# Kernel optimization log

Measured on AMD Instinct MI355X. Metric: run time of the kernel, lower is better.

Reference implementation:

```python
import jax, jax.numpy as jnp
import numpy as np

B, T, C = 4, 8192, 1024
H, D = 16, 64  # n_head, head_dim


def setup_inputs() -> dict:
    key = jax.random.key(0)
    ks = jax.random.split(key, 9)
    s = 1.0 / np.sqrt(C)
    return {
        "x": jax.random.normal(ks[0], (B, T, C), jnp.float32),
        "Wq": jax.random.uniform(ks[1], (C, C), jnp.float32, -s, s),
        "bq": jax.random.uniform(ks[2], (C,), jnp.float32, -s, s),
        "Wk": jax.random.uniform(ks[3], (C, C), jnp.float32, -s, s),
        "bk": jax.random.uniform(ks[4], (C,), jnp.float32, -s, s),
        "Wv": jax.random.uniform(ks[5], (C, C), jnp.float32, -s, s),
        "bv": jax.random.uniform(ks[6], (C,), jnp.float32, -s, s),
        "Wp": jax.random.uniform(ks[7], (C, C), jnp.float32, -s, s),
        "bp": jax.random.uniform(ks[8], (C,), jnp.float32, -s, s),
    }


def _heads(t):
    # (B,T,C) -> (B,H,T,D)
    return t.reshape(B, T, H, D).transpose(0, 2, 1, 3)


def reference(x, Wq, bq, Wk, bk, Wv, bv, Wp, bp):
    q = _heads(x @ Wq.T + bq)
    k = _heads(x @ Wk.T + bk)
    v = _heads(x @ Wv.T + bv)
    # attn_type='l1': softmax q,k over feature dim; L1 normalizer
    q = jax.nn.softmax(q, axis=-1)
    k = jax.nn.softmax(k, axis=-1)
    k_sum = k.sum(axis=-2, keepdims=True)               # (B,H,1,D)
    D_inv = 1.0 / (q * k_sum).sum(axis=-1, keepdims=True)  # (B,H,T,1)
    context = jnp.einsum('bhtd,bhte->bhde', k, v)       # (B,H,D,D)
    out = jnp.einsum('bhtd,bhde->bhte', q, context) * D_inv + q
    out = out.transpose(0, 2, 1, 3).reshape(B, T, C)
    return out @ Wp.T + bp
```

## Files before the change

kernel.cpp:

```cpp
#include <hip/hip_runtime.h>
#include <hip/hip_bf16.h>
#include <stdint.h>


#define BT    32768
#define CDIM  1024

using bf16 = __hip_bfloat16;
typedef short  short8   __attribute__((ext_vector_type(8)));
typedef short  short4_t __attribute__((ext_vector_type(4)));
typedef unsigned short ushort4_t __attribute__((ext_vector_type(4)));
typedef float  floatx4  __attribute__((ext_vector_type(4)));

__device__ __forceinline__ float bfbits2f(unsigned short u) {
    union { unsigned int i; float f; } c; c.i = ((unsigned int)u) << 16; return c.f;
}

__device__ __forceinline__ void gld_lds16(const void* g, void* lds) {
    __builtin_amdgcn_global_load_lds(
        (const __attribute__((address_space(1))) uint32_t*)g,
        (__attribute__((address_space(3))) uint32_t*)lds,
        16, 0, 0);
}

__global__ void zero_kernel(float* __restrict__ p) {
    p[(size_t)blockIdx.x * 256 + threadIdx.x] = 0.0f;
}

__global__ void cvt_kernel(const float* __restrict__ x,
                           const float* __restrict__ Wq, const float* __restrict__ Wk,
                           const float* __restrict__ Wv, const float* __restrict__ Wp,
                           bf16* __restrict__ xb, bf16* __restrict__ Wb) {
    const int XF4 = (BT * CDIM) / 4;
    int i = blockIdx.x * 256 + threadIdx.x;
    const float* src; bf16* dst; int off;
    if (i < XF4) { src = x; dst = xb; off = i; }
    else {
        int i2 = i - XF4;
        int wi = i2 >> 18;
        off = i2 & 0x3FFFF;
        src = (wi == 0) ? Wq : (wi == 1) ? Wk : (wi == 2) ? Wv : Wp;
        dst = Wb + (size_t)wi * 1048576;
    }
    float4 f = ((const float4*)src)[off];
    union { bf16 h[4]; short4_t v; } u;
    u.h[0] = __float2bfloat16(f.x); u.h[1] = __float2bfloat16(f.y);
    u.h[2] = __float2bfloat16(f.z); u.h[3] = __float2bfloat16(f.w);
    *(short4_t*)(dst + (size_t)off * 4) = u.v;
}


__device__ __forceinline__ short8 frag_ld(const bf16* hb, int r, int s4q) {
    return *(const short8*)(hb + r * 64 + (((s4q) ^ (r & 7)) << 3));
}

__device__ __forceinline__ void stage_half(const bf16* g, bf16* l, int tid) {
    int ln = tid & 63, w = tid >> 6;
    int r = w * 8 + (ln >> 3);
    int c = ((ln & 7) ^ (ln >> 3)) << 3;
    gld_lds16(g + (size_t)r * CDIM + c, l + w * 512);
    gld_lds16(g + (size_t)(r + 64) * CDIM + c, l + 4096 + w * 512);
}

#define MFMA16(a, b, c) __builtin_amdgcn_mfma_f32_16x16x32_bf16(a, b, c, 0, 0, 0)

__device__ __forceinline__ void pipe256(const bf16* __restrict__ Ab,
                                        const bf16* __restrict__ Bb,
                                        bf16* ldsA, bf16* ldsB,
                                        int tid, floatx4 acc[8][4]) {
    const int lane = tid & 63;
    const int wv = tid >> 6;
    const int quad = lane >> 4, l15 = lane & 15;
    const int wm = wv >> 2, wn = wv & 3;
    const int rA0 = wm * 64 + l15;
    const int rB0 = (wn & 1) * 64 + l15;
    const bf16* ldsBh = ldsB + (wn >> 1) * 8192;
    short8 bfr[4][2];

#define STAGE_A(b, h, kt) stage_half(Ab + (size_t)((h) * 128) * CDIM + (kt) * 64, \
                                     ldsA + (b) * 16384 + (h) * 8192, tid)
#define STAGE_B(b, h, kt) stage_half(Bb + (size_t)((h) * 128) * CDIM + (kt) * 64, \
                                     ldsB + (b) * 16384 + (h) * 8192, tid)
#define VMW(n) asm volatile("s_waitcnt vmcnt(" #n ")" ::: "memory")
#define VM_NONE

#define QPHASE(BUF, QA, MM, LOADB, STG, VMC) do {                              \
    const bf16* aH_ = ldsA + (BUF) * 16384 + (QA) * 8192;                      \
    short8 a00_ = frag_ld(aH_, rA0 + (MM) * 32,      quad);                    \
    short8 a01_ = frag_ld(aH_, rA0 + (MM) * 32,      4 + quad);                \
    short8 a10_ = frag_ld(aH_, rA0 + (MM) * 32 + 16, quad);                    \
    short8 a11_ = frag_ld(aH_, rA0 + (MM) * 32 + 16, 4 + quad);                \
    if (LOADB) {                                                               \
        const bf16* bH_ = ldsBh + (BUF) * 16384;                               \
        _Pragma("unroll")                                                      \
        for (int j = 0; j < 4; ++j) {                                          \
            bfr[j][0] = frag_ld(bH_, rB0 + j * 16, quad);                      \
            bfr[j][1] = frag_ld(bH_, rB0 + j * 16, 4 + quad);                  \
        }                                                                      \
    }                                                                          \
    STG; VMC;                                                                  \
    __builtin_amdgcn_s_barrier();                                              \
    asm volatile("s_waitcnt lgkmcnt(0)" ::: "memory");                         \
    __builtin_amdgcn_s_setprio(1);                                             \
    _Pragma("unroll")                                                          \
    for (int j = 0; j < 4; ++j) {                                              \
        acc[(QA)*4+(MM)*2  ][j] = MFMA16(a00_, bfr[j][0], acc[(QA)*4+(MM)*2  ][j]); \
        acc[(QA)*4+(MM)*2  ][j] = MFMA16(a01_, bfr[j][1], acc[(QA)*4+(MM)*2  ][j]); \
        acc[(QA)*4+(MM)*2+1][j] = MFMA16(a10_, bfr[j][0], acc[(QA)*4+(MM)*2+1][j]); \
        acc[(QA)*4+(MM)*2+1][j] = MFMA16(a11_, bfr[j][1], acc[(QA)*4+(MM)*2+1][j]); \
    }                                                                          \
    __builtin_amdgcn_s_setprio(0);                                             \
    __builtin_amdgcn_s_barrier();                                              \
} while (0)

    STAGE_B(0, 0, 0); STAGE_B(0, 1, 0); STAGE_A(0, 0, 0); STAGE_A(0, 1, 0);
    STAGE_B(1, 0, 1); STAGE_B(1, 1, 1); STAGE_A(1, 0, 1);
    VMW(8);
    __builtin_amdgcn_s_barrier();

    #pragma unroll 1
    for (int i = 0; i < 7; ++i) {
        int t = 2 * i;
        QPHASE(0, 0, 0, 1, STAGE_A(1, 1, t + 1), VM_NONE);
        QPHASE(0, 0, 1, 0, STAGE_B(0, 0, t + 2), VMW(10));
        QPHASE(0, 1, 0, 0, STAGE_B(0, 1, t + 2), VM_NONE);
        QPHASE(0, 1, 1, 0, STAGE_A(0, 0, t + 2), VMW(8));
        QPHASE(1, 0, 0, 1, STAGE_A(0, 1, t + 2), VM_NONE);
        QPHASE(1, 0, 1, 0, STAGE_B(1, 0, t + 3), VMW(10));
        QPHASE(1, 1, 0, 0, STAGE_B(1, 1, t + 3), VM_NONE);
        QPHASE(1, 1, 1, 0, STAGE_A(1, 0, t + 3), VMW(8));
    }
    QPHASE(0, 0, 0, 1, STAGE_A(1, 1, 15), VM_NONE);
    QPHASE(0, 0, 1, 0, VM_NONE, VMW(8));
    QPHASE(0, 1, 0, 0, VM_NONE, VM_NONE);
    QPHASE(0, 1, 1, 0, VM_NONE, VMW(2));
    QPHASE(1, 0, 0, 1, VM_NONE, VM_NONE);
    QPHASE(1, 0, 1, 0, VM_NONE, VMW(0));
    QPHASE(1, 1, 0, 0, VM_NONE, VM_NONE);
    QPHASE(1, 1, 1, 0, VM_NONE, VM_NONE);

#undef QPHASE
#undef STAGE_A
#undef STAGE_B
}

__global__ __launch_bounds__(512, 2)
void gemm_qkv(const bf16* __restrict__ A, const bf16* __restrict__ Bw,
              const float* __restrict__ bq, const float* __restrict__ bk,
              const float* __restrict__ bv,
              bf16* __restrict__ qb, bf16* __restrict__ kb, bf16* __restrict__ vb) {
    __shared__ bf16 ldsA[32768];
    __shared__ bf16 ldsB[32768];
    int tid = threadIdx.x;
    int bid = blockIdx.x;
    int swz = (bid & 7) * 192 + (bid >> 3);
    int bn = swz % 12, bm = swz / 12;

    floatx4 acc[8][4] = {};
    pipe256(A + (size_t)bm * 256 * CDIM, Bw + (size_t)bn * 256 * CDIM,
            ldsA, ldsB, tid, acc);

    int lane = tid & 63, wv = tid >> 6, quad = lane >> 4, l15 = lane & 15;
    int wm = wv >> 2, wn = wv & 3;
    int n_abs = bn * 256 + wn * 64;
    bf16* dst; const float* biasp; int ncol0; bool smax;
    if (n_abs < 1024)      { dst = qb; biasp = bq; ncol0 = n_abs;        smax = true;  }
    else if (n_abs < 2048) { dst = kb; biasp = bk; ncol0 = n_abs - 1024; smax = true;  }
    else                   { dst = vb; biasp = bv; ncol0 = n_abs - 2048; smax = false; }
    float bias4[4];
    #pragma unroll
    for (int j = 0; j < 4; ++j) bias4[j] = biasp[ncol0 + j * 16 + l15];
    size_t row0 = (size_t)bm * 256 + wm * 64;

    #pragma unroll
    for (int i = 0; i < 8; ++i) {
        #pragma unroll
        for (int r = 0; r < 4; ++r) {
            float vals[4];
            #pragma unroll
            for (int j = 0; j < 4; ++j) vals[j] = acc[i][j][r] + bias4[j];
            if (smax) {
                float mx = fmaxf(fmaxf(vals[0], vals[1]), fmaxf(vals[2], vals[3]));
                #pragma unroll
                for (int d = 1; d < 16; d <<= 1) mx = fmaxf(mx, __shfl_xor(mx, d));
                float s = 0.f;
                #pragma unroll
                for (int j = 0; j < 4; ++j) { vals[j] = __expf(vals[j] - mx); s += vals[j]; }
                #pragma unroll
                for (int d = 1; d < 16; d <<= 1) s += __shfl_xor(s, d);
                float rinv = 1.0f / s;
                #pragma unroll
                for (int j = 0; j < 4; ++j) vals[j] *= rinv;
            }
            size_t row = row0 + ((i >> 2) * 128) + ((i & 3) * 16) + quad * 4 + r;
            #pragma unroll
            for (int j = 0; j < 4; ++j)
                dst[row * 1024 + ncol0 + j * 16 + l15] = __float2bfloat16(vals[j]);
        }
    }
}

__global__ __launch_bounds__(256)
void ctx_kernel(const bf16* __restrict__ kbuf, const bf16* __restrict__ vbuf,
                float* __restrict__ ctx, float* __restrict__ ksum) {
    int bid = blockIdx.x;
    int head = bid >> 4, chunk = bid & 15;
    int b = head >> 4, h = head & 15;
    size_t rowbase = (size_t)b * 8192 + (size_t)chunk * 512;
    int coff = h * 64;
    __shared__ bf16 ks[64 * 64];
    __shared__ bf16 vs[64 * 64];
    int tid = threadIdx.x;
    int lrow = tid >> 2, lpart = tid & 3;
    int di = tid >> 4, ei = tid & 15;

    float acc[16];
    #pragma unroll
    for (int i = 0; i < 16; ++i) acc[i] = 0.f;
    float ksv[4] = {0.f, 0.f, 0.f, 0.f};

    size_t gbase = (rowbase + lrow) * 1024 + coff + lpart * 16;
    short8 pk0 = *(const short8*)(kbuf + gbase);
    short8 pk1 = *(const short8*)(kbuf + gbase + 8);
    short8 pv0 = *(const short8*)(vbuf + gbase);
    short8 pv1 = *(const short8*)(vbuf + gbase + 8);

    for (int st = 0; st < 8; ++st) {
        __syncthreads();
        *(short8*)&ks[lrow * 64 + lpart * 16]     = pk0;
        *(short8*)&ks[lrow * 64 + lpart * 16 + 8] = pk1;
        *(short8*)&vs[lrow * 64 + lpart * 16]     = pv0;
        *(short8*)&vs[lrow * 64 + lpart * 16 + 8] = pv1;
        __syncthreads();
        if (st < 7) {
            size_t g = gbase + (size_t)(st + 1) * 64 * 1024;
            pk0 = *(const short8*)(kbuf + g);
            pk1 = *(const short8*)(kbuf + g + 8);
            pv0 = *(const short8*)(vbuf + g);
            pv1 = *(const short8*)(vbuf + g + 8);
        }
        for (int t = 0; t < 64; ++t) {
            ushort4_t ku = *(const ushort4_t*)&ks[t * 64 + di * 4];
            ushort4_t vu = *(const ushort4_t*)&vs[t * 64 + ei * 4];
            float kd[4], ve[4];
            #pragma unroll
            for (int i = 0; i < 4; ++i) { kd[i] = bfbits2f(ku[i]); ve[i] = bfbits2f(vu[i]); }
            #pragma unroll
            for (int i = 0; i < 4; ++i)
                #pragma unroll
                for (int j = 0; j < 4; ++j)
                    acc[i * 4 + j] = fmaf(kd[i], ve[j], acc[i * 4 + j]);
            #pragma unroll
            for (int j = 0; j < 4; ++j) ksv[j] += kd[j];
        }
    }
    float* cptr = ctx + (size_t)head * 4096;
    #pragma unroll
    for (int i = 0; i < 4; ++i)
        #pragma unroll
        for (int j = 0; j < 4; ++j)
            atomicAdd(&cptr[(di * 4 + i) * 64 + ei * 4 + j], acc[i * 4 + j]);
    if (ei == 0) {
        #pragma unroll
        for (int j = 0; j < 4; ++j) atomicAdd(&ksum[head * 64 + di * 4 + j], ksv[j]);
    }
}

#define QS 72
__global__ __launch_bounds__(256)
void attn_kernel(const bf16* __restrict__ qbuf, const float* __restrict__ ctx,
                 const float* __restrict__ ksum, bf16* __restrict__ ab) {
    int bid = blockIdx.x;
    int head = bid >> 7, tb = bid & 127;
    int b = head >> 4, h = head & 15;
    size_t row0 = (size_t)b * 8192 + (size_t)tb * 64;
    int coff = h * 64;
    __shared__ bf16 qs[64 * QS];
    __shared__ bf16 cts[64 * QS];
    __shared__ float ksums[64];
    __shared__ float dinv[64];
    int tid = threadIdx.x, lane = tid & 63, wv = tid >> 6;

    {
        int lrow = tid >> 2, lpart = tid & 3;
        size_t g = (row0 + lrow) * 1024 + coff + lpart * 16;
        short8 q0 = *(const short8*)(qbuf + g);
        short8 q1 = *(const short8*)(qbuf + g + 8);
        *(short8*)&qs[lrow * QS + lpart * 16]     = q0;
        *(short8*)&qs[lrow * QS + lpart * 16 + 8] = q1;
    }
    {
        const float* cp = ctx + (size_t)head * 4096;
        #pragma unroll
        for (int it = 0; it < 4; ++it) {
            int fi = it * 256 + tid;
            int d = fi >> 4, e0 = (fi & 15) * 4;
            float4 f = ((const float4*)cp)[fi];
            cts[(e0 + 0) * QS + d] = __float2bfloat16(f.x);
            cts[(e0 + 1) * QS + d] = __float2bfloat16(f.y);
            cts[(e0 + 2) * QS + d] = __float2bfloat16(f.z);
            cts[(e0 + 3) * QS + d] = __float2bfloat16(f.w);
        }
    }
    if (tid < 64) ksums[tid] = ksum[head * 64 + tid];
    __syncthreads();

    {
        int t = tid >> 2, dg = tid & 3;
        float p = 0.f;
        #pragma unroll
        for (int j = 0; j < 16; ++j)
            p = fmaf(__bfloat162float(qs[t * QS + dg * 16 + j]), ksums[dg * 16 + j], p);
        p += __shfl_xor(p, 1);
        p += __shfl_xor(p, 2);
        if (dg == 0) dinv[t] = 1.0f / p;
    }
    __syncthreads();

    int quad = lane >> 4, l15 = lane & 15;
    int trow0 = wv * 16;
    short8 aF0 = *(const short8*)&qs[(trow0 + l15) * QS + quad * 8];
    short8 aF1 = *(const short8*)&qs[(trow0 + l15) * QS + 32 + quad * 8];
    floatx4 acc[4] = {};
    #pragma unroll
    for (int ni = 0; ni < 4; ++ni) {
        short8 b0 = *(const short8*)&cts[(ni * 16 + l15) * QS + quad * 8];
        short8 b1 = *(const short8*)&cts[(ni * 16 + l15) * QS + 32 + quad * 8];
        acc[ni] = __builtin_amdgcn_mfma_f32_16x16x32_bf16(aF0, b0, acc[ni], 0, 0, 0);
        acc[ni] = __builtin_amdgcn_mfma_f32_16x16x32_bf16(aF1, b1, acc[ni], 0, 0, 0);
    }
    float dv[4];
    #pragma unroll
    for (int r = 0; r < 4; ++r) dv[r] = dinv[trow0 + quad * 4 + r];
    #pragma unroll
    for (int ni = 0; ni < 4; ++ni) {
        #pragma unroll
        for (int r = 0; r < 4; ++r) {
            int row = trow0 + quad * 4 + r;
            int col = ni * 16 + l15;
            float val = acc[ni][r] * dv[r] + __bfloat162float(qs[row * QS + col]);
            ab[(row0 + row) * 1024 + coff + col] = __float2bfloat16(val);
        }
    }
}

__global__ __launch_bounds__(512, 2)
void gemm_out(const bf16* __restrict__ A, const bf16* __restrict__ Bw,
              const float* __restrict__ bp, float* __restrict__ outp) {
    __shared__ bf16 ldsA[32768];
    __shared__ bf16 ldsB[32768];
    int tid = threadIdx.x;
    int bid = blockIdx.x;
    int swz = (bid & 7) * 64 + (bid >> 3);
    int bn = swz & 3, bm = swz >> 2;

    floatx4 acc[8][4] = {};
    pipe256(A + (size_t)bm * 256 * CDIM, Bw + (size_t)bn * 256 * CDIM,
            ldsA, ldsB, tid, acc);

    int lane = tid & 63, wv = tid >> 6, quad = lane >> 4, l15 = lane & 15;
    int wm = wv >> 2, wn = wv & 3;
    int gcol0 = bn * 256 + wn * 64;
    float bias4[4];
    #pragma unroll
    for (int j = 0; j < 4; ++j) bias4[j] = bp[gcol0 + j * 16 + l15];
    size_t row0 = (size_t)bm * 256 + wm * 64;

    #pragma unroll
    for (int i = 0; i < 8; ++i) {
        #pragma unroll
        for (int r = 0; r < 4; ++r) {
            size_t row = row0 + ((i >> 2) * 128) + ((i & 3) * 16) + quad * 4 + r;
            #pragma unroll
            for (int j = 0; j < 4; ++j)
                outp[row * 1024 + gcol0 + j * 16 + l15] = acc[i][j][r] + bias4[j];
        }
    }
}

extern "C" void kernel_launch(void* const* d_in, const int* in_sizes, int n_in,
                              void* d_out, int out_size, void* d_ws, size_t ws_size,
                              hipStream_t stream) {
    const float* x  = (const float*)d_in[0];
    const float* Wq = (const float*)d_in[1];
    const float* bq = (const float*)d_in[2];
    const float* Wk = (const float*)d_in[3];
    const float* bk = (const float*)d_in[4];
    const float* Wv = (const float*)d_in[5];
    const float* bv = (const float*)d_in[6];
    const float* Wp = (const float*)d_in[7];
    const float* bp = (const float*)d_in[8];
    float* outp = (float*)d_out;

    char* ws = (char*)d_ws;
    bf16*  xb   = (bf16*)(ws);
    bf16*  Wb   = (bf16*)(ws + 67108864);
    bf16*  qb   = (bf16*)(ws + 75497472);
    bf16*  kb   = (bf16*)(ws + 142606336);
    bf16*  vb   = (bf16*)(ws + 209715200);
    float* ctx  = (float*)(ws + 276824064);
    float* ksum = (float*)(ws + 277872640);
    bf16*  ab   = (bf16*)(ws);

    zero_kernel<<<1040, 256, 0, stream>>>(ctx);
    cvt_kernel<<<36864, 256, 0, stream>>>(x, Wq, Wk, Wv, Wp, xb, Wb);
    gemm_qkv<<<1536, 512, 0, stream>>>(xb, Wb, bq, bk, bv, qb, kb, vb);
    ctx_kernel<<<1024, 256, 0, stream>>>(kb, vb, ctx, ksum);
    attn_kernel<<<8192, 256, 0, stream>>>(qb, ctx, ksum, ab);
    gemm_out<<<512, 512, 0, stream>>>(ab, Wb + (size_t)3072 * 1024, bp, outp);
}
```

Before: 691.3 us.

## Compute K^T V context with MFMA via transposed swizzled LDS tiles

The context kernel previously computed the per-head D×D K^T·V outer-product sum with scalar FMAs on bf16 values read from LDS. It now stores K and V tiles transposed (d-major) in LDS with an XOR swizzle and uses 16x16x32 bf16 MFMA instructions to accumulate the context, with the k_sum reduction folded into the staging loop and reduced through shuffles and a shared buffer. This removes scalar FMA and LDS-read overhead, at the cost of scalar 2-byte transposed LDS writes and more complex indexing. The gemm_out kernel and macros are only moved in the file.

```diff
diff --git a/kernel.cpp b/kernel.cpp
--- a/kernel.cpp
+++ b/kernel.cpp
@@ -63,6 +63,8 @@
 }
 
 #define MFMA16(a, b, c) __builtin_amdgcn_mfma_f32_16x16x32_bf16(a, b, c, 0, 0, 0)
+#define VMW(n) asm volatile("s_waitcnt vmcnt(" #n ")" ::: "memory")
+#define VM_NONE
 
 __device__ __forceinline__ void pipe256(const bf16* __restrict__ Ab,
                                         const bf16* __restrict__ Bb,
@@ -81,8 +83,6 @@
                                      ldsA + (b) * 16384 + (h) * 8192, tid)
 #define STAGE_B(b, h, kt) stage_half(Bb + (size_t)((h) * 128) * CDIM + (kt) * 64, \
                                      ldsB + (b) * 16384 + (h) * 8192, tid)
-#define VMW(n) asm volatile("s_waitcnt vmcnt(" #n ")" ::: "memory")
-#define VM_NONE
 
 #define QPHASE(BUF, QA, MM, LOADB, STG, VMC) do {                              \
     const bf16* aH_ = ldsA + (BUF) * 16384 + (QA) * 8192;                      \
@@ -200,6 +200,40 @@
     }
 }
 
+__global__ __launch_bounds__(512, 2)
+void gemm_out(const bf16* __restrict__ A, const bf16* __restrict__ Bw,
+              const float* __restrict__ bp, float* __restrict__ outp) {
+    __shared__ bf16 ldsA[32768];
+    __shared__ bf16 ldsB[32768];
+    int tid = threadIdx.x;
+    int bid = blockIdx.x;
+    int swz = (bid & 7) * 64 + (bid >> 3);
+    int bn = swz & 3, bm = swz >> 2;
+
+    floatx4 acc[8][4] = {};
+    pipe256(A + (size_t)bm * 256 * CDIM, Bw + (size_t)bn * 256 * CDIM,
+            ldsA, ldsB, tid, acc);
+
+    int lane = tid & 63, wv = tid >> 6, quad = lane >> 4, l15 = lane & 15;
+    int wm = wv >> 2, wn = wv & 3;
+    int gcol0 = bn * 256 + wn * 64;
+    float bias4[4];
+    #pragma unroll
+    for (int j = 0; j < 4; ++j) bias4[j] = bp[gcol0 + j * 16 + l15];
+    size_t row0 = (size_t)bm * 256 + wm * 64;
+
+    #pragma unroll
+    for (int i = 0; i < 8; ++i) {
+        #pragma unroll
+        for (int r = 0; r < 4; ++r) {
+            size_t row = row0 + ((i >> 2) * 128) + ((i & 3) * 16) + quad * 4 + r;
+            #pragma unroll
+            for (int j = 0; j < 4; ++j)
+                outp[row * 1024 + gcol0 + j * 16 + l15] = acc[i][j][r] + bias4[j];
+        }
+    }
+}
+
 __global__ __launch_bounds__(256)
 void ctx_kernel(const bf16* __restrict__ kbuf, const bf16* __restrict__ vbuf,
                 float* __restrict__ ctx, float* __restrict__ ksum) {
@@ -208,62 +242,80 @@
     int b = head >> 4, h = head & 15;
     size_t rowbase = (size_t)b * 8192 + (size_t)chunk * 512;
     int coff = h * 64;
-    __shared__ bf16 ks[64 * 64];
-    __shared__ bf16 vs[64 * 64];
-    int tid = threadIdx.x;
-    int lrow = tid >> 2, lpart = tid & 3;
-    int di = tid >> 4, ei = tid & 15;
-
-    float acc[16];
-    #pragma unroll
-    for (int i = 0; i < 16; ++i) acc[i] = 0.f;
-    float ksv[4] = {0.f, 0.f, 0.f, 0.f};
-
-    size_t gbase = (rowbase + lrow) * 1024 + coff + lpart * 16;
-    short8 pk0 = *(const short8*)(kbuf + gbase);
-    short8 pk1 = *(const short8*)(kbuf + gbase + 8);
-    short8 pv0 = *(const short8*)(vbuf + gbase);
-    short8 pv1 = *(const short8*)(vbuf + gbase + 8);
-
+    __shared__ unsigned short kT[4096];
+    __shared__ unsigned short vT[4096];
+    __shared__ float ksum_s[64];
+    int tid = threadIdx.x, lane = tid & 63, wv = tid >> 6;
+    int quad = lane >> 4, l15 = lane & 15;
+    int c8 = tid & 7, trow = tid >> 3;
+    if (tid < 64) ksum_s[tid] = 0.f;
+
+    float kacc[8] = {0.f, 0.f, 0.f, 0.f, 0.f, 0.f, 0.f, 0.f};
+    floatx4 acc4[4] = {};
+
+    size_t g0 = (rowbase + trow) * 1024 + coff + c8 * 8;
+    short8 pk0 = *(const short8*)(kbuf + g0);
+    short8 pk1 = *(const short8*)(kbuf + g0 + 32 * 1024);
+    short8 pv0 = *(const short8*)(vbuf + g0);
+    short8 pv1 = *(const short8*)(vbuf + g0 + 32 * 1024);
+
+    int tb0 = trow >> 3;
     for (int st = 0; st < 8; ++st) {
         __syncthreads();
-        *(short8*)&ks[lrow * 64 + lpart * 16]     = pk0;
-        *(short8*)&ks[lrow * 64 + lpart * 16 + 8] = pk1;
-        *(short8*)&vs[lrow * 64 + lpart * 16]     = pv0;
-        *(short8*)&vs[lrow * 64 + lpart * 16 + 8] = pv1;
+        #pragma unroll
+        for (int j = 0; j < 8; ++j) {
+            int d = c8 * 8 + j;
+            int base = d * 64 + (trow & 7);
+            int sw0 = (tb0 ^ j ^ c8) << 3;
+            int sw1 = ((tb0 + 4) ^ j ^ c8) << 3;
+            unsigned short ku0 = (unsigned short)((short*)&pk0)[j];
+            unsigned short ku1 = (unsigned short)((short*)&pk1)[j];
+            kT[base + sw0] = ku0;
+            kT[base + sw1] = ku1;
+            vT[base + sw0] = (unsigned short)((short*)&pv0)[j];
+            vT[base + sw1] = (unsigned short)((short*)&pv1)[j];
+            kacc[j] += bfbits2f(ku0) + bfbits2f(ku1);
+        }
         __syncthreads();
         if (st < 7) {
-            size_t g = gbase + (size_t)(st + 1) * 64 * 1024;
+            size_t g = g0 + (size_t)(st + 1) * 64 * 1024;
             pk0 = *(const short8*)(kbuf + g);
-            pk1 = *(const short8*)(kbuf + g + 8);
+            pk1 = *(const short8*)(kbuf + g + 32 * 1024);
             pv0 = *(const short8*)(vbuf + g);
-            pv1 = *(const short8*)(vbuf + g + 8);
-        }
-        for (int t = 0; t < 64; ++t) {
-            ushort4_t ku = *(const ushort4_t*)&ks[t * 64 + di * 4];
-            ushort4_t vu = *(const ushort4_t*)&vs[t * 64 + ei * 4];
-            float kd[4], ve[4];
+            pv1 = *(const short8*)(vbuf + g + 32 * 1024);
+        }
+        #pragma unroll
+        for (int ks = 0; ks < 2; ++ks) {
+            int dA = wv * 16 + l15;
+            int blkA = (ks * 4 + quad) ^ (dA & 7) ^ (dA >> 3);
+            short8 aF = *(const short8*)&kT[dA * 64 + (blkA << 3)];
             #pragma unroll
-            for (int i = 0; i < 4; ++i) { kd[i] = bfbits2f(ku[i]); ve[i] = bfbits2f(vu[i]); }
-            #pragma unroll
-            for (int i = 0; i < 4; ++i)
-                #pragma unroll
-                for (int j = 0; j < 4; ++j)
-                    acc[i * 4 + j] = fmaf(kd[i], ve[j], acc[i * 4 + j]);
-            #pragma unroll
-            for (int j = 0; j < 4; ++j) ksv[j] += kd[j];
-        }
+            for (int n = 0; n < 4; ++n) {
+                int eB = n * 16 + l15;
+                int blkB = (ks * 4 + quad) ^ (eB & 7) ^ (eB >> 3);
+                short8 bF = *(const short8*)&vT[eB * 64 + (blkB << 3)];
+                acc4[n] = MFMA16(aF, bF, acc4[n]);
+            }
+        }
+    }
+
+    #pragma unroll
+    for (int j = 0; j < 8; ++j) {
+        float v = kacc[j];
+        v += __shfl_xor(v, 8); v += __shfl_xor(v, 16); v += __shfl_xor(v, 32);
+        if (lane < 8) atomicAdd(&ksum_s[lane * 8 + j], v);
     }
     float* cptr = ctx + (size_t)head * 4096;
     #pragma unroll
-    for (int i = 0; i < 4; ++i)
-        #pragma unroll
-        for (int j = 0; j < 4; ++j)
-            atomicAdd(&cptr[(di * 4 + i) * 64 + ei * 4 + j], acc[i * 4 + j]);
-    if (ei == 0) {
-        #pragma unroll
-        for (int j = 0; j < 4; ++j) atomicAdd(&ksum[head * 64 + di * 4 + j], ksv[j]);
-    }
+    for (int n = 0; n < 4; ++n)
+        #pragma unroll
+        for (int rr = 0; rr < 4; ++rr) {
+            int d = wv * 16 + quad * 4 + rr;
+            int e = n * 16 + l15;
+            atomicAdd(&cptr[d * 64 + e], acc4[n][rr]);
+        }
+    __syncthreads();
+    if (tid < 64) atomicAdd(&ksum[head * 64 + tid], ksum_s[tid]);
 }
 
 #define QS 72
@@ -344,40 +396,6 @@
     }
 }
 
-__global__ __launch_bounds__(512, 2)
-void gemm_out(const bf16* __restrict__ A, const bf16* __restrict__ Bw,
-              const float* __restrict__ bp, float* __restrict__ outp) {
-    __shared__ bf16 ldsA[32768];
-    __shared__ bf16 ldsB[32768];
-    int tid = threadIdx.x;
-    int bid = blockIdx.x;
-    int swz = (bid & 7) * 64 + (bid >> 3);
-    int bn = swz & 3, bm = swz >> 2;
-
-    floatx4 acc[8][4] = {};
-    pipe256(A + (size_t)bm * 256 * CDIM, Bw + (size_t)bn * 256 * CDIM,
-            ldsA, ldsB, tid, acc);
-
-    int lane = tid & 63, wv = tid >> 6, quad = lane >> 4, l15 = lane & 15;
-    int wm = wv >> 2, wn = wv & 3;
-    int gcol0 = bn * 256 + wn * 64;
-    float bias4[4];
-    #pragma unroll
-    for (int j = 0; j < 4; ++j) bias4[j] = bp[gcol0 + j * 16 + l15];
-    size_t row0 = (size_t)bm * 256 + wm * 64;
-
-    #pragma unroll
-    for (int i = 0; i < 8; ++i) {
-        #pragma unroll
-        for (int r = 0; r < 4; ++r) {
-            size_t row = row0 + ((i >> 2) * 128) + ((i & 3) * 16) + quad * 4 + r;
-            #pragma unroll
-            for (int j = 0; j < 4; ++j)
-                outp[row * 1024 + gcol0 + j * 16 + l15] = acc[i][j][r] + bias4[j];
-        }
-    }
-}
-
 extern "C" void kernel_launch(void* const* d_in, const int* in_sizes, int n_in,
                               void* d_out, int out_size, void* d_ws, size_t ws_size,
                               hipStream_t stream) {
```

After: 646.7 us. 1.07x faster.
